# Performance work log

Hardware: AMD Instinct MI355X
Metric: run time of the kernel (lower is better)

The kernel has to match this reference:

```python
import jax, jax.numpy as jnp
import numpy as np

HEAD_SIZE = 64
NUM_HEADS = 8
D_IN = 512

def setup_inputs() -> dict:
    key = jax.random.key(0)
    ks = jax.random.split(key, 6)
    B, Nq, Nk = 4, 2048, 2048
    HD = HEAD_SIZE * NUM_HEADS
    q = jax.random.normal(ks[0], (B, Nq, D_IN), dtype=jnp.float32)
    k = jax.random.normal(ks[1], (B, Nk, D_IN), dtype=jnp.float32)
    s = 1.0 / np.sqrt(D_IN)
    Wq = jax.random.normal(ks[2], (D_IN, HD), dtype=jnp.float32) * s
    Wk = jax.random.normal(ks[3], (D_IN, HD), dtype=jnp.float32) * s
    Wv = jax.random.normal(ks[4], (D_IN, HD), dtype=jnp.float32) * s
    Wh = jax.random.normal(ks[5], (HD, HEAD_SIZE), dtype=jnp.float32) * (1.0 / np.sqrt(HD))
    return {"q": q, "k": k, "Wq": Wq, "Wk": Wk, "Wv": Wv, "Wh": Wh}

def reference(q, k, Wq, Wk, Wv, Wh):
    B, Nq, _ = q.shape
    Nk = k.shape[1]
    H, hs = NUM_HEADS, HEAD_SIZE
    # QKV projections (no bias), reshape to [B, H, N, hs]
    q_ = (q @ Wq).reshape(B, Nq, H, hs).transpose(0, 2, 1, 3)
    k_ = (k @ Wk).reshape(B, Nk, H, hs).transpose(0, 2, 1, 3)
    v_ = (k @ Wv).reshape(B, Nk, H, hs).transpose(0, 2, 1, 3)
    scale = 1.0 / jnp.sqrt(jnp.float32(hs))
    score = jnp.einsum('bhqd,bhkd->bhqk', q_, k_) * scale  # [B,H,Nq,Nk]
    attn = jax.nn.softmax(score, axis=-1)
    wv = jnp.einsum('bhqk,bhkd->bhqd', attn, v_)  # [B,H,Nq,hs]
    wv = wv.transpose(0, 2, 1, 3).reshape(B, Nq, H * hs)
    return wv @ Wh  # [B, Nq, hs]
```

## Files before the change

### kernel.cpp

```cpp
#include <hip/hip_runtime.h>
#include <hip/hip_bf16.h>

#define BB   4
#define NQ   2048
#define NKK  2048
#define DIN  512
#define NH   8
#define HS   64
#define HD   512

typedef __hip_bfloat16 bf16;
typedef unsigned short ushort_t;
typedef __attribute__((ext_vector_type(8))) short short8;
typedef __attribute__((ext_vector_type(4))) float f32x4;
typedef __attribute__((ext_vector_type(16))) float f32x16;
typedef __attribute__((ext_vector_type(4))) unsigned u32x4;

__device__ __forceinline__ unsigned short f2bu(float x) {
  bf16 h = __float2bfloat16(x);
  return *(unsigned short*)&h;
}

__global__ __launch_bounds__(256) void wtrans_kernel(
    const float* __restrict__ Wq, const float* __restrict__ Wk,
    const float* __restrict__ Wv, const float* __restrict__ Wh,
    ushort_t* __restrict__ Wt, ushort_t* __restrict__ Wht) {
  const int z = blockIdx.z;
  const float* src;
  ushort_t* dst;
  int S;
  if (z < 3) {
    src = (z == 0) ? Wq : (z == 1) ? Wk : Wv;
    dst = Wt + (size_t)z * 512 * 512;
    S = 512;
  } else {
    if (blockIdx.y != 0) return;
    src = Wh;
    dst = Wht;
    S = 64;
  }
  const int k0 = blockIdx.x * 64;
  const int n0 = (z < 3) ? blockIdx.y * 64 : 0;

  __shared__ ushort_t Ls[64 * 72];
  const int tid = threadIdx.x;
  {
    int r = tid >> 2, cb = (tid & 3) * 16;
    const float* sp = src + (size_t)(k0 + r) * S + n0 + cb;
#pragma unroll
    for (int ii = 0; ii < 4; ++ii) {
      float4 f = *(const float4*)(sp + ii * 4);
      __align__(8) ushort_t t4[4] = {f2bu(f.x), f2bu(f.y), f2bu(f.z), f2bu(f.w)};
      *(uint2*)(&Ls[r * 72 + cb + ii * 4]) = *(uint2*)t4;
    }
  }
  __syncthreads();
  {
    int rr = tid >> 2, tb = (tid & 3) * 16;
    __align__(16) ushort_t tmp[16];
#pragma unroll
    for (int j = 0; j < 16; ++j) tmp[j] = Ls[(tb + j) * 72 + rr];
    ushort_t* dp = dst + (size_t)(n0 + rr) * 512 + k0 + tb;
    *(int4*)dp       = ((int4*)tmp)[0];
    *(int4*)(dp + 8) = ((int4*)tmp)[1];
  }
}

__global__ __launch_bounds__(256) void proj_kernel(
    const float* __restrict__ q, const float* __restrict__ k,
    const ushort_t* __restrict__ Wt, ushort_t* __restrict__ Qf,
    ushort_t* __restrict__ Kf, ushort_t* __restrict__ Vf) {
  const int z = blockIdx.z;
  const float* X = (z == 0) ? q : k;
  const ushort_t* Wz = Wt + (size_t)z * 512 * 512;
  ushort_t* Y = (z == 0) ? Qf : (z == 1) ? Kf : Vf;
  const float sc = (z == 0) ? 0.18033688011112042f : 1.0f;

  __shared__ ushort_t As[2 * 128 * 40];
  __shared__ ushort_t Bs[2 * 128 * 40];

  const int tid  = threadIdx.x;
  const int lane = tid & 63;
  const int w    = tid >> 6;
  const int quad = lane >> 4;
  const int c    = lane & 15;
  const int wm   = w >> 1, wn = w & 1;

  const int m0 = blockIdx.y * 128;
  const int n0 = blockIdx.x * 128;
  const int sm  = tid >> 1;
  const int skb = (tid & 1) * 16;

  float4 xa[4];
  int4 wb[2];
  auto load_t = [&](int k0) {
    const float* xp = X + (size_t)(m0 + sm) * DIN + k0 + skb;
    xa[0] = *(const float4*)(xp + 0);
    xa[1] = *(const float4*)(xp + 4);
    xa[2] = *(const float4*)(xp + 8);
    xa[3] = *(const float4*)(xp + 12);
    const ushort_t* wp = Wz + (size_t)(n0 + sm) * 512 + k0 + skb;
    wb[0] = *(const int4*)wp;
    wb[1] = *(const int4*)(wp + 8);
  };
  auto store_t = [&](int buf) {
    __align__(16) ushort_t ta[16];
#pragma unroll
    for (int ii = 0; ii < 4; ++ii) {
      ta[ii * 4 + 0] = f2bu(xa[ii].x);
      ta[ii * 4 + 1] = f2bu(xa[ii].y);
      ta[ii * 4 + 2] = f2bu(xa[ii].z);
      ta[ii * 4 + 3] = f2bu(xa[ii].w);
    }
    *(int4*)(&As[buf * 5120 + sm * 40 + skb])     = ((int4*)ta)[0];
    *(int4*)(&As[buf * 5120 + sm * 40 + skb + 8]) = ((int4*)ta)[1];
    *(int4*)(&Bs[buf * 5120 + sm * 40 + skb])     = wb[0];
    *(int4*)(&Bs[buf * 5120 + sm * 40 + skb + 8]) = wb[1];
  };

  f32x4 acc[4][4];
#pragma unroll
  for (int m = 0; m < 4; ++m)
#pragma unroll
    for (int n = 0; n < 4; ++n) acc[m][n] = (f32x4)0.0f;

  load_t(0);
  store_t(0);
  __syncthreads();

  for (int t = 0; t < 16; ++t) {
    const int cur = t & 1;
    if (t < 15) load_t((t + 1) * 32);
    const ushort_t* as = As + cur * 5120;
    const ushort_t* bs = Bs + cur * 5120;
    short8 af[4], bfr[4];
#pragma unroll
    for (int m = 0; m < 4; ++m)
      af[m] = *(const short8*)(&as[(wm * 64 + m * 16 + c) * 40 + quad * 8]);
#pragma unroll
    for (int n = 0; n < 4; ++n)
      bfr[n] = *(const short8*)(&bs[(wn * 64 + n * 16 + c) * 40 + quad * 8]);
#pragma unroll
    for (int m = 0; m < 4; ++m)
#pragma unroll
      for (int n = 0; n < 4; ++n)
        acc[m][n] = __builtin_amdgcn_mfma_f32_16x16x32_bf16(af[m], bfr[n], acc[m][n], 0, 0, 0);
    if (t < 15) store_t(cur ^ 1);
    __syncthreads();
  }

#pragma unroll
  for (int m = 0; m < 4; ++m)
#pragma unroll
    for (int n = 0; n < 4; ++n)
#pragma unroll
      for (int r = 0; r < 4; ++r) {
        int row = m0 + wm * 64 + m * 16 + quad * 4 + r;
        int col = n0 + wn * 64 + n * 16 + c;
        Y[(size_t)row * HD + col] = f2bu(acc[m][n][r] * sc);
      }
}

__global__ __launch_bounds__(256) void vtrans_kernel(
    const ushort_t* __restrict__ Vf, ushort_t* __restrict__ Vt) {
  const int b  = blockIdx.z;
  const int t0 = blockIdx.x * 64;
  const int c0 = blockIdx.y * 64;
  __shared__ ushort_t Ls[64 * 72];
  const int tid = threadIdx.x;
  {
    int r = tid >> 2, cb = (tid & 3) * 16;
    const ushort_t* src = Vf + (size_t)(b * NQ + t0 + r) * HD + c0 + cb;
    *(int4*)(&Ls[r * 72 + cb])     = *(const int4*)src;
    *(int4*)(&Ls[r * 72 + cb + 8]) = *(const int4*)(src + 8);
  }
  __syncthreads();
  {
    int rr = tid >> 2, tb = (tid & 3) * 16;
    __align__(16) ushort_t tmp[16];
#pragma unroll
    for (int j = 0; j < 16; ++j) tmp[j] = Ls[(tb + j) * 72 + rr];
    ushort_t* dst = Vt + (size_t)(b * HD + c0 + rr) * NKK + t0 + tb;
    *(int4*)dst       = ((int4*)tmp)[0];
    *(int4*)(dst + 8) = ((int4*)tmp)[1];
  }
}

__global__ __launch_bounds__(64, 1) void attn_kernel(
    const ushort_t* __restrict__ Qf, const ushort_t* __restrict__ Kf,
    const ushort_t* __restrict__ Vt, ushort_t* __restrict__ CTX) {
  const int id   = blockIdx.x;
  const int xcd  = id & 7;
  const int slot = id >> 3;
  const int p    = xcd * 4 + (slot >> 5);
  const int qb   = slot & 31;
  const int h    = p & 7;
  const int b    = p >> 3;

  __shared__ ushort_t Kt[2][4096];
  __shared__ ushort_t Vs[2][4096];

  const int lane = threadIdx.x & 63;
  const int ql   = lane & 31;
  const int hi   = lane >> 5;

  const int q0 = qb * 64;

  short8 bq[2][4];
#pragma unroll
  for (int qs = 0; qs < 2; ++qs) {
    const ushort_t* qp =
        Qf + (size_t)(b * NQ + q0 + qs * 32 + ql) * HD + h * HS + hi * 8;
#pragma unroll
    for (int ks = 0; ks < 4; ++ks) bq[qs][ks] = *(const short8*)(qp + ks * 16);
  }

  const int sub  = lane >> 3;
  const int slt  = lane & 7;
  const int csrc = slt ^ sub;
  const ushort_t* kp0 =
      Kf + (size_t)(b * NKK + sub) * HD + h * HS + csrc * 8;
  const ushort_t* vp0 =
      Vt + (size_t)((b * NH + h) * HS + sub) * NKK + csrc * 8;

  auto stage = [&](int buf, int kt) {
    const ushort_t* kp = kp0 + (size_t)kt * 64 * HD;
    const ushort_t* vp = vp0 + (size_t)kt * 64;
#pragma unroll
    for (int i = 0; i < 8; ++i) {
      __builtin_amdgcn_global_load_lds(
          (const __attribute__((address_space(1))) unsigned*)(kp + (size_t)i * 8 * HD),
          (__attribute__((address_space(3))) unsigned*)(&Kt[buf][i * 512]),
          16, 0, 0);
      __builtin_amdgcn_global_load_lds(
          (const __attribute__((address_space(1))) unsigned*)(vp + (size_t)i * 8 * NKK),
          (__attribute__((address_space(3))) unsigned*)(&Vs[buf][i * 512]),
          16, 0, 0);
    }
  };

  f32x16 o[2][2];
#pragma unroll
  for (int qs = 0; qs < 2; ++qs)
#pragma unroll
    for (int ng = 0; ng < 2; ++ng) o[qs][ng] = (f32x16)0.0f;
  float lsum[2] = {0.0f, 0.0f};

  stage(0, 0);

  for (int t = 0; t < NKK / 64; ++t) {
    const int buf = t & 1;
    if (t < NKK / 64 - 1) {
      stage(buf ^ 1, t + 1);
      asm volatile("s_waitcnt vmcnt(16)" ::: "memory");
    } else {
      asm volatile("s_waitcnt vmcnt(0)" ::: "memory");
    }
    const ushort_t* kb = &Kt[buf][0];
    const ushort_t* vb = &Vs[buf][0];

    short8 ak[2][4], bv[2][4];
#pragma unroll
    for (int kg = 0; kg < 2; ++kg) {
      const int krow = kg * 32 + ql;
#pragma unroll
      for (int ks = 0; ks < 4; ++ks)
        ak[kg][ks] = *(const short8*)(&kb[krow * 64 + (((ks * 2 + hi) ^ (krow & 7)) * 8)]);
    }
#pragma unroll
    for (int ng = 0; ng < 2; ++ng) {
      const int vrow = ng * 32 + ql;
#pragma unroll
      for (int ks = 0; ks < 4; ++ks)
        bv[ng][ks] = *(const short8*)(&vb[vrow * 64 + (((ks * 2 + hi) ^ (vrow & 7)) * 8)]);
    }

#pragma unroll
    for (int kg = 0; kg < 2; ++kg) {
      f32x16 s[2];
      s[0] = (f32x16)0.0f;
      s[1] = (f32x16)0.0f;
      __builtin_amdgcn_s_setprio(1);
#pragma unroll
      for (int ks = 0; ks < 4; ++ks) {
        s[0] = __builtin_amdgcn_mfma_f32_32x32x16_bf16(ak[kg][ks], bq[0][ks], s[0], 0, 0, 0);
        s[1] = __builtin_amdgcn_mfma_f32_32x32x16_bf16(ak[kg][ks], bq[1][ks], s[1], 0, 0, 0);
      }
      __builtin_amdgcn_s_setprio(0);

      short8 pa[2][2];
#pragma unroll
      for (int qs = 0; qs < 2; ++qs) {
        float p_[16];
#pragma unroll
        for (int r = 0; r < 16; ++r) p_[r] = __builtin_amdgcn_exp2f(s[qs][r]);
        {
          float a0 = p_[0] + p_[1], a1 = p_[2] + p_[3], a2 = p_[4] + p_[5], a3 = p_[6] + p_[7];
          float a4 = p_[8] + p_[9], a5 = p_[10] + p_[11], a6 = p_[12] + p_[13], a7 = p_[14] + p_[15];
          a0 += a1; a2 += a3; a4 += a5; a6 += a7;
          lsum[qs] += (a0 + a2) + (a4 + a6);
        }
#pragma unroll
        for (int sp = 0; sp < 2; ++sp) {
          unsigned wA, wB, wC, wD;
          asm("v_cvt_pk_bf16_f32 %0, %1, %2" : "=v"(wA) : "v"(p_[8 * sp + 0]), "v"(p_[8 * sp + 1]));
          asm("v_cvt_pk_bf16_f32 %0, %1, %2" : "=v"(wB) : "v"(p_[8 * sp + 2]), "v"(p_[8 * sp + 3]));
          asm("v_cvt_pk_bf16_f32 %0, %1, %2" : "=v"(wC) : "v"(p_[8 * sp + 4]), "v"(p_[8 * sp + 5]));
          asm("v_cvt_pk_bf16_f32 %0, %1, %2" : "=v"(wD) : "v"(p_[8 * sp + 6]), "v"(p_[8 * sp + 7]));
          asm("v_permlane32_swap_b32 %0, %1" : "+v"(wA), "+v"(wC));
          asm("v_permlane32_swap_b32 %0, %1" : "+v"(wB), "+v"(wD));
          u32x4 pw;
          pw.x = wA;
          pw.y = wB;
          pw.z = wC;
          pw.w = wD;
          pa[qs][sp] = __builtin_bit_cast(short8, pw);
        }
      }

      __builtin_amdgcn_s_setprio(1);
#pragma unroll
      for (int sp = 0; sp < 2; ++sp) {
        const int ks = kg * 2 + sp;
#pragma unroll
        for (int ng = 0; ng < 2; ++ng) {
          o[0][ng] = __builtin_amdgcn_mfma_f32_32x32x16_bf16(pa[0][sp], bv[ng][ks], o[0][ng], 0, 0, 0);
          o[1][ng] = __builtin_amdgcn_mfma_f32_32x32x16_bf16(pa[1][sp], bv[ng][ks], o[1][ng], 0, 0, 0);
        }
      }
      __builtin_amdgcn_s_setprio(0);
    }
  }

  float inv[2];
#pragma unroll
  for (int qs = 0; qs < 2; ++qs) {
    float tot = lsum[qs] + __shfl_xor(lsum[qs], 32);
    inv[qs] = 1.0f / tot;
  }

#pragma unroll
  for (int qs = 0; qs < 2; ++qs)
#pragma unroll
    for (int r = 0; r < 16; ++r) {
      int qr = (r & 3) + 8 * (r >> 2) + 4 * hi;
      float iv = __shfl(inv[qs], qr);
      size_t base = (size_t)(b * NQ + q0 + qs * 32 + qr) * HD + h * HS + ql;
      CTX[base]      = f2bu(o[qs][0][r] * iv);
      CTX[base + 32] = f2bu(o[qs][1][r] * iv);
    }
}

__global__ __launch_bounds__(64) void outproj_kernel(
    const ushort_t* __restrict__ CTX, const ushort_t* __restrict__ Wht,
    float* __restrict__ out) {
  const int lane = threadIdx.x & 63;
  const int quad = lane >> 4, c = lane & 15;
  const int m0 = blockIdx.x * 16;

  f32x4 o[4];
#pragma unroll
  for (int n = 0; n < 4; ++n) o[n] = (f32x4)0.0f;

  const ushort_t* arow = CTX + (size_t)(m0 + c) * HD;
#pragma unroll 4
  for (int ks = 0; ks < 16; ++ks) {
    short8 a = *(const short8*)(arow + ks * 32 + quad * 8);
#pragma unroll
    for (int nd = 0; nd < 4; ++nd) {
      short8 bn = *(const short8*)(Wht + (size_t)(nd * 16 + c) * 512 + ks * 32 + quad * 8);
      o[nd] = __builtin_amdgcn_mfma_f32_16x16x32_bf16(a, bn, o[nd], 0, 0, 0);
    }
  }
#pragma unroll
  for (int nd = 0; nd < 4; ++nd)
#pragma unroll
    for (int r = 0; r < 4; ++r)
      out[(size_t)(m0 + quad * 4 + r) * HS + nd * 16 + c] = o[nd][r];
}

extern "C" void kernel_launch(void* const* d_in, const int* in_sizes, int n_in,
                              void* d_out, int out_size, void* d_ws,
                              size_t ws_size, hipStream_t stream) {
  const float* q  = (const float*)d_in[0];
  const float* k  = (const float*)d_in[1];
  const float* Wq = (const float*)d_in[2];
  const float* Wk = (const float*)d_in[3];
  const float* Wv = (const float*)d_in[4];
  const float* Wh = (const float*)d_in[5];
  float* out = (float*)d_out;

  const size_t E = (size_t)BB * NQ * HD;
  ushort_t* ws  = (ushort_t*)d_ws;
  ushort_t* Qf  = ws;
  ushort_t* Kf  = Qf + E;
  ushort_t* Vt  = Kf + E;
  ushort_t* CTX = Vt + E;
  ushort_t* Vf  = CTX + E;
  ushort_t* Wt  = Vf + E;
  ushort_t* Wht = Wt + (size_t)3 * 512 * 512;

  wtrans_kernel<<<dim3(8, 8, 4), 256, 0, stream>>>(Wq, Wk, Wv, Wh, Wt, Wht);
  proj_kernel<<<dim3(HD / 128, BB * NQ / 128, 3), 256, 0, stream>>>(
      q, k, Wt, Qf, Kf, Vf);
  vtrans_kernel<<<dim3(NKK / 64, HD / 64, BB), 256, 0, stream>>>(Vf, Vt);
  attn_kernel<<<dim3(32 * NH * BB), 64, 0, stream>>>(Qf, Kf, Vt, CTX);
  outproj_kernel<<<dim3(BB * NQ / 16), 64, 0, stream>>>(CTX, Wht, out);
}
```

Measured before the change: 199.1 us.

## Fuse V transpose into projection epilogue and drop setprio in attention

The V projection now writes its output directly in transposed layout from the MFMA accumulators, so the separate vtrans kernel and the Vf round-trip through global memory are removed. The transposed stores write 4 contiguous bf16 values per lane along the sequence dimension, which may be less coalesced than the old row-major writes. Separately, the s_setprio raise and lower around the MFMA blocks in the attention kernel are removed.

```diff
diff --git a/kernel.cpp b/kernel.cpp
--- a/kernel.cpp
+++ b/kernel.cpp
@@ -69,11 +69,10 @@
 __global__ __launch_bounds__(256) void proj_kernel(
     const float* __restrict__ q, const float* __restrict__ k,
     const ushort_t* __restrict__ Wt, ushort_t* __restrict__ Qf,
-    ushort_t* __restrict__ Kf, ushort_t* __restrict__ Vf) {
+    ushort_t* __restrict__ Kf, ushort_t* __restrict__ Vt) {
   const int z = blockIdx.z;
   const float* X = (z == 0) ? q : k;
   const ushort_t* Wz = Wt + (size_t)z * 512 * 512;
-  ushort_t* Y = (z == 0) ? Qf : (z == 1) ? Kf : Vf;
   const float sc = (z == 0) ? 0.18033688011112042f : 1.0f;
 
   __shared__ ushort_t As[2 * 128 * 40];
@@ -149,40 +148,31 @@
     __syncthreads();
   }
 
-#pragma unroll
-  for (int m = 0; m < 4; ++m)
-#pragma unroll
-    for (int n = 0; n < 4; ++n)
-#pragma unroll
-      for (int r = 0; r < 4; ++r) {
-        int row = m0 + wm * 64 + m * 16 + quad * 4 + r;
-        int col = n0 + wn * 64 + n * 16 + c;
-        Y[(size_t)row * HD + col] = f2bu(acc[m][n][r] * sc);
+  if (z != 2) {
+    ushort_t* Y = (z == 0) ? Qf : Kf;
+#pragma unroll
+    for (int m = 0; m < 4; ++m)
+#pragma unroll
+      for (int n = 0; n < 4; ++n)
+#pragma unroll
+        for (int r = 0; r < 4; ++r) {
+          int row = m0 + wm * 64 + m * 16 + quad * 4 + r;
+          int col = n0 + wn * 64 + n * 16 + c;
+          Y[(size_t)row * HD + col] = f2bu(acc[m][n][r] * sc);
+        }
+  } else {
+#pragma unroll
+    for (int m = 0; m < 4; ++m)
+#pragma unroll
+      for (int n = 0; n < 4; ++n) {
+        int row0 = m0 + wm * 64 + m * 16 + quad * 4;
+        int col  = n0 + wn * 64 + n * 16 + c;
+        int bb   = row0 >> 11;
+        int t0   = row0 & 2047;
+        __align__(8) ushort_t t4[4] = {f2bu(acc[m][n][0]), f2bu(acc[m][n][1]),
+                                       f2bu(acc[m][n][2]), f2bu(acc[m][n][3])};
+        *(uint2*)(&Vt[((size_t)bb * HD + col) * NKK + t0]) = *(uint2*)t4;
       }
-}
-
-__global__ __launch_bounds__(256) void vtrans_kernel(
-    const ushort_t* __restrict__ Vf, ushort_t* __restrict__ Vt) {
-  const int b  = blockIdx.z;
-  const int t0 = blockIdx.x * 64;
-  const int c0 = blockIdx.y * 64;
-  __shared__ ushort_t Ls[64 * 72];
-  const int tid = threadIdx.x;
-  {
-    int r = tid >> 2, cb = (tid & 3) * 16;
-    const ushort_t* src = Vf + (size_t)(b * NQ + t0 + r) * HD + c0 + cb;
-    *(int4*)(&Ls[r * 72 + cb])     = *(const int4*)src;
-    *(int4*)(&Ls[r * 72 + cb + 8]) = *(const int4*)(src + 8);
-  }
-  __syncthreads();
-  {
-    int rr = tid >> 2, tb = (tid & 3) * 16;
-    __align__(16) ushort_t tmp[16];
-#pragma unroll
-    for (int j = 0; j < 16; ++j) tmp[j] = Ls[(tb + j) * 72 + rr];
-    ushort_t* dst = Vt + (size_t)(b * HD + c0 + rr) * NKK + t0 + tb;
-    *(int4*)dst       = ((int4*)tmp)[0];
-    *(int4*)(dst + 8) = ((int4*)tmp)[1];
   }
 }
 
@@ -280,13 +270,11 @@
       f32x16 s[2];
       s[0] = (f32x16)0.0f;
       s[1] = (f32x16)0.0f;
-      __builtin_amdgcn_s_setprio(1);
 #pragma unroll
       for (int ks = 0; ks < 4; ++ks) {
         s[0] = __builtin_amdgcn_mfma_f32_32x32x16_bf16(ak[kg][ks], bq[0][ks], s[0], 0, 0, 0);
         s[1] = __builtin_amdgcn_mfma_f32_32x32x16_bf16(ak[kg][ks], bq[1][ks], s[1], 0, 0, 0);
       }
-      __builtin_amdgcn_s_setprio(0);
 
       short8 pa[2][2];
 #pragma unroll
@@ -318,7 +306,6 @@
         }
       }
 
-      __builtin_amdgcn_s_setprio(1);
 #pragma unroll
       for (int sp = 0; sp < 2; ++sp) {
         const int ks = kg * 2 + sp;
@@ -328,7 +315,6 @@
           o[1][ng] = __builtin_amdgcn_mfma_f32_32x32x16_bf16(pa[1][sp], bv[ng][ks], o[1][ng], 0, 0, 0);
         }
       }
-      __builtin_amdgcn_s_setprio(0);
     }
   }
 
@@ -402,8 +388,7 @@
 
   wtrans_kernel<<<dim3(8, 8, 4), 256, 0, stream>>>(Wq, Wk, Wv, Wh, Wt, Wht);
   proj_kernel<<<dim3(HD / 128, BB * NQ / 128, 3), 256, 0, stream>>>(
-      q, k, Wt, Qf, Kf, Vf);
-  vtrans_kernel<<<dim3(NKK / 64, HD / 64, BB), 256, 0, stream>>>(Vf, Vt);
+      q, k, Wt, Qf, Kf, Vt);
   attn_kernel<<<dim3(32 * NH * BB), 64, 0, stream>>>(Qf, Kf, Vt, CTX);
   outproj_kernel<<<dim3(BB * NQ / 16), 64, 0, stream>>>(CTX, Wht, out);
 }
```

Result: faster. 191.7 us (-3.7%).
